# Kernel optimization log

Hardware: AMD Instinct MI355X
Metric: run time of the kernel (lower is better)

The kernel has to match this reference:

```python
import jax, jax.numpy as jnp
import numpy as np

N_STREAMS = 8
DIM = 1024
N_HEADS = 16
HEAD_DIM = DIM // N_HEADS
STREAM_DIM = DIM // N_STREAMS
EPS = 1e-6


def setup_inputs() -> dict:
    key = jax.random.key(0)
    ks = jax.random.split(key, 20)
    B, S, D = 2, 2048, DIM
    inp = {
        "x": jax.random.normal(ks[0], (B, S, D), jnp.float32),
        "rope_cos": jax.random.uniform(ks[1], (S, HEAD_DIM), jnp.float32),
        "rope_sin": jax.random.uniform(ks[2], (S, HEAD_DIM), jnp.float32),
        # DeltaOperator: learned per-channel decay logits
        "delta_decay": jax.random.normal(ks[3], (D,), jnp.float32) * 0.02,
        # gate_proj: Linear(D, 3*n)
        "gate_w": jax.random.normal(ks[4], (3 * N_STREAMS, D), jnp.float32) * 0.02,
        "gate_b": jnp.zeros((3 * N_STREAMS,), jnp.float32),
        "phi_res": jax.random.normal(ks[5], (N_STREAMS, N_STREAMS), jnp.float32) * 0.02,
        "ln1_w": jnp.ones((D,), jnp.float32),
        "ln2_w": jnp.ones((D,), jnp.float32),
        # MLP (StrategicLinear == Linear at inference)
        "w1": jax.random.normal(ks[6], (4 * D, D), jnp.float32) * 0.02,
        "b1": jnp.zeros((4 * D,), jnp.float32),
        "w2": jax.random.normal(ks[7], (D, 4 * D), jnp.float32) * 0.02,
        "b2": jnp.zeros((D,), jnp.float32),
        # nn.MultiheadAttention params
        "in_proj_w": jax.random.normal(ks[8], (3 * D, D), jnp.float32) * 0.02,
        "in_proj_b": jnp.zeros((3 * D,), jnp.float32),
        "out_w": jax.random.normal(ks[9], (D, D), jnp.float32) * 0.02,
        "out_b": jnp.zeros((D,), jnp.float32),
    }
    return inp


def delta_operator(x, decay_logits):
    # out_t = x_t - s_{t-1};  s_t = beta*s_{t-1} + (1-beta)*x_t  (per-channel EMA delta)
    beta = jax.nn.sigmoid(decay_logits)  # [D]

    def step(s, xt):
        out = xt - s
        s_new = beta * s + (1.0 - beta) * xt
        return s_new, out

    xT = jnp.swapaxes(x, 0, 1)  # [S,B,D]
    s0 = jnp.zeros_like(xT[0])
    _, ysT = jax.lax.scan(step, s0, xT)
    return jnp.swapaxes(ysT, 0, 1)  # [B,S,D]


def rms_norm(x, w):
    var = jnp.mean(x * x, axis=-1, keepdims=True)
    return x * jax.lax.rsqrt(var + EPS) * w


def sinkhorn_knopp(phi, iterations=15):
    K = jnp.exp(phi)
    for _ in range(iterations):
        K = K / jnp.sum(K, axis=1, keepdims=True)
        K = K / jnp.sum(K, axis=0, keepdims=True)
    return K


def causal_mha(x, in_proj_w, in_proj_b, out_w, out_b):
    B, S, D = x.shape
    qkv = x @ in_proj_w.T + in_proj_b  # [B,S,3D]
    q, k, v = jnp.split(qkv, 3, axis=-1)
    def heads(t):
        return t.reshape(B, S, N_HEADS, HEAD_DIM).transpose(0, 2, 1, 3)  # [B,H,S,hd]
    q, k, v = heads(q), heads(k), heads(v)
    scores = jnp.einsum("bhqd,bhkd->bhqk", q, k) / jnp.sqrt(jnp.float32(HEAD_DIM))
    mask = jnp.tril(jnp.ones((S, S), bool))
    scores = jnp.where(mask, scores, jnp.float32(-1e9))
    attn = jax.nn.softmax(scores, axis=-1)
    o = jnp.einsum("bhqk,bhkd->bhqd", attn, v)
    o = o.transpose(0, 2, 1, 3).reshape(B, S, D)
    return o @ out_w.T + out_b


def reference(x, rope_cos, rope_sin, delta_decay, gate_w, gate_b, phi_res,
              ln1_w, ln2_w, w1, b1, w2, b2, in_proj_w, in_proj_b, out_w, out_b):
    B, S, D = x.shape
    n = N_STREAMS
    x_delta = delta_operator(x, delta_decay)
    x_state = jnp.mean(x_delta, axis=1)  # [B,D]
    gates = x_state @ gate_w.T + gate_b  # [B,3n]
    g_res = jax.nn.sigmoid(gates[:, 2 * n:])[:, None, :, None]  # [B,1,n,1]
    H_res = sinkhorn_knopp(phi_res, 15)
    x_streams = x_delta.reshape(B, S, n, STREAM_DIM)
    # (x_perm @ H.T).permute back == einsum over stream axis
    mhc_out = jnp.einsum("bsnd,mn->bsmd", x_streams * g_res, H_res).reshape(B, S, D)
    normed = rms_norm(x_delta, ln1_w)
    attn_out = causal_mha(normed, in_proj_w, in_proj_b, out_w, out_b)
    normed2 = rms_norm(x_delta + attn_out, ln2_w)
    h = jax.nn.gelu(normed2 @ w1.T + b1, approximate=False)
    ffn_out = h @ w2.T + b2
    return x_delta + attn_out + ffn_out + mhc_out
```

## Files before the change

kernel.cpp:

```cpp
#include <hip/hip_runtime.h>
#include <hip/hip_bf16.h>
#include <math.h>

#define BB 2
#define SS 2048
#define DDIM 1024
#define NHEAD 16
#define NSTR 8
#define SDIMC 128
#define NCH 16
#define CLEN 128
#define EPSV 1e-6f

using bf16 = __hip_bfloat16;
typedef __attribute__((ext_vector_type(8))) __bf16 bf8;
typedef __attribute__((ext_vector_type(4))) __bf16 bf4v;
typedef __attribute__((ext_vector_type(4))) float f4;

__device__ __forceinline__ bf16 f2b(float v) { return __float2bfloat16(v); }
__device__ __forceinline__ bf8 ld8(const bf16* p) { return *(const bf8*)p; }
__device__ __forceinline__ f4 MFMA(bf8 a, bf8 b, f4 c) {
  return __builtin_amdgcn_mfma_f32_16x16x32_bf16(a, b, c, 0, 0, 0);
}
__device__ __forceinline__ float sigm(float x) { return 1.0f / (1.0f + expf(-x)); }
__device__ __forceinline__ float fexp2(float x) { return __builtin_amdgcn_exp2f(x); }
__device__ __forceinline__ float max3f(float a, float b, float c) {
  return fmaxf(fmaxf(a, b), c);
}

__device__ __forceinline__ float gelu_f(float v) {
  float x = v * 0.70710678118654752f;
  float ax = fabsf(x);
  float t = __builtin_amdgcn_rcpf(1.0f + 0.3275911f * ax);
  float p = ((((1.061405429f * t - 1.453152027f) * t + 1.421413741f) * t
              - 0.284496736f) * t + 0.254829592f) * t;
  float e = 1.0f - p * fexp2(-ax * ax * 1.4426950408889634f);
  e = copysignf(e, x);
  return 0.5f * v * (1.0f + e);
}

__device__ __forceinline__ void glds16(bf16* l, const bf16* g) {
  __builtin_amdgcn_global_load_lds(
      (const __attribute__((address_space(1))) unsigned int*)g,
      (__attribute__((address_space(3))) unsigned int*)l, 16, 0, 0);
}

__global__ __launch_bounds__(256) void cvt_all(const float* __restrict__ ipw,
                                               const float* __restrict__ ow,
                                               const float* __restrict__ w1,
                                               const float* __restrict__ w2,
                                               bf16* __restrict__ WIPW,
                                               bf16* __restrict__ WOW,
                                               bf16* __restrict__ W1B,
                                               bf16* __restrict__ W2B) {
  const int S1 = 3 * DDIM * DDIM, S2 = S1 + DDIM * DDIM,
            S3 = S2 + 4 * DDIM * DDIM;
  int i4 = (blockIdx.x * 256 + threadIdx.x) * 4;
  const float* src;
  bf16* dst;
  int off;
  if (i4 < S1)      { src = ipw; dst = WIPW; off = i4; }
  else if (i4 < S2) { src = ow;  dst = WOW;  off = i4 - S1; }
  else if (i4 < S3) { src = w1;  dst = W1B;  off = i4 - S2; }
  else              { src = w2;  dst = W2B;  off = i4 - S3; }
  float4 v = *(const float4*)(src + off);
  bf4v o;
  o[0] = (__bf16)v.x; o[1] = (__bf16)v.y; o[2] = (__bf16)v.z; o[3] = (__bf16)v.w;
  *(bf4v*)(dst + off) = o;
}

__global__ __launch_bounds__(256) void delta_passA(const float* __restrict__ x,
                                                   const float* __restrict__ decay,
                                                   float* __restrict__ SA) {
  int idx = blockIdx.x * 256 + threadIdx.x;
  int d = idx % DDIM;
  int c = (idx / DDIM) % NCH;
  int b = idx / (DDIM * NCH);
  float beta = sigm(decay[d]);
  float omb = 1.0f - beta;
  const float* xp = x + ((size_t)(b * SS + c * CLEN)) * DDIM + d;
  float s = 0.0f;
  for (int j = 0; j < CLEN; j++) {
    float xv = xp[(size_t)j * DDIM];
    s = beta * s + omb * xv;
  }
  SA[idx] = s;
}

__global__ __launch_bounds__(256) void delta_passB(const float* __restrict__ SA,
                                                   const float* __restrict__ decay,
                                                   float* __restrict__ SIN) {
  int idx = blockIdx.x * 256 + threadIdx.x;
  int d = idx % DDIM;
  int b = idx / DDIM;
  float beta = sigm(decay[d]);
  float p = beta;
  for (int i = 0; i < 7; i++) p *= p;
  float s = 0.0f;
  for (int c = 0; c < NCH; c++) {
    SIN[(b * NCH + c) * DDIM + d] = s;
    s = p * s + SA[(b * NCH + c) * DDIM + d];
  }
}

__global__ __launch_bounds__(256) void delta_passC(const float* __restrict__ x,
                                                   const float* __restrict__ decay,
                                                   const float* __restrict__ SIN,
                                                   float* __restrict__ XD,
                                                   float* __restrict__ SA) {
  int idx = blockIdx.x * 256 + threadIdx.x;
  int d = idx % DDIM;
  int c = (idx / DDIM) % NCH;
  int b = idx / (DDIM * NCH);
  float beta = sigm(decay[d]);
  float omb = 1.0f - beta;
  const float* xp = x + ((size_t)(b * SS + c * CLEN)) * DDIM + d;
  float* xdp = XD + ((size_t)(b * SS + c * CLEN)) * DDIM + d;
  float s = SIN[idx];
  float sum = 0.0f;
  for (int j = 0; j < CLEN; j++) {
    float xv = xp[(size_t)j * DDIM];
    float o = xv - s;
    xdp[(size_t)j * DDIM] = o;
    sum += o;
    s = beta * s + omb * xv;
  }
  SA[idx] = sum;
}

__global__ __launch_bounds__(1024) void gates_sinkhorn(const float* __restrict__ SA,
                                                       const float* __restrict__ gw,
                                                       const float* __restrict__ gb,
                                                       const float* __restrict__ phi,
                                                       float* __restrict__ gres,
                                                       float* __restrict__ hres) {
  int tid = threadIdx.x;
  int wave = tid >> 6, lane = tid & 63;
  int b = wave >> 3, j = wave & 7;
  float acc = 0.0f;
  for (int d = lane; d < DDIM; d += 64) {
    float xs = 0.0f;
    for (int c = 0; c < NCH; c++) xs += SA[(b * NCH + c) * DDIM + d];
    xs *= (1.0f / (float)SS);
    acc += xs * gw[(2 * NSTR + j) * DDIM + d];
  }
  for (int off = 32; off > 0; off >>= 1) acc += __shfl_down(acc, off);
  if (lane == 0) gres[b * NSTR + j] = sigm(acc + gb[2 * NSTR + j]);
  __syncthreads();
  if (tid == 0) {
    float Km[8][8];
    for (int i = 0; i < 8; i++)
      for (int jj = 0; jj < 8; jj++) Km[i][jj] = expf(phi[i * 8 + jj]);
    for (int it = 0; it < 15; it++) {
      for (int i = 0; i < 8; i++) {
        float rs = 0.0f;
        for (int jj = 0; jj < 8; jj++) rs += Km[i][jj];
        float inv = 1.0f / rs;
        for (int jj = 0; jj < 8; jj++) Km[i][jj] *= inv;
      }
      for (int jj = 0; jj < 8; jj++) {
        float cs = 0.0f;
        for (int i = 0; i < 8; i++) cs += Km[i][jj];
        float inv = 1.0f / cs;
        for (int i = 0; i < 8; i++) Km[i][jj] *= inv;
      }
    }
    for (int i = 0; i < 8; i++)
      for (int jj = 0; jj < 8; jj++) hres[i * 8 + jj] = Km[i][jj];
  }
}

__global__ __launch_bounds__(256) void rmsnorm_k(const float* __restrict__ in,
                                                 const float* __restrict__ w,
                                                 bf16* __restrict__ out) {
  int row = blockIdx.x;
  const float* r = in + (size_t)row * DDIM;
  int tid = threadIdx.x;
  float ss = 0.0f;
  for (int i = tid; i < DDIM; i += 256) {
    float v = r[i];
    ss += v * v;
  }
  for (int off = 32; off > 0; off >>= 1) ss += __shfl_down(ss, off);
  __shared__ float red[4];
  if ((tid & 63) == 0) red[tid >> 6] = ss;
  __syncthreads();
  float tot = red[0] + red[1] + red[2] + red[3];
  float sc = rsqrtf(tot / (float)DDIM + EPSV);
  bf16* o = out + (size_t)row * DDIM;
  for (int i = tid; i < DDIM; i += 256) o[i] = f2b(r[i] * sc * w[i]);
}

template <int EPI>
__global__ __launch_bounds__(512, 2) void gemm256(const bf16* __restrict__ Ag,
                                                  const bf16* __restrict__ Wg,
                                                  const float* __restrict__ bias,
                                                  bf16* __restrict__ outp,
                                                  int M, int N, int K, int nby) {
  __shared__ __align__(16) bf16 As[2][16384];
  __shared__ __align__(16) bf16 Bs[2][16384];
  int nwg = gridDim.x;
  int cpx = nwg >> 3;
  int l = (blockIdx.x & 7) * cpx + (blockIdx.x >> 3);
  int bm = l / nby, bn = l % nby;
  int m0 = bm * 256, n0 = bn * 256;
  int tid = threadIdx.x;
  int lane = tid & 63, wv = tid >> 6;
  int ml = lane & 15, quad = lane >> 4;
  int wrow = wv >> 2, wcol = wv & 3;

  size_t aoff[2][2], boff[2][2];
  int lof[2][2];
#pragma unroll
  for (int h = 0; h < 2; h++)
#pragma unroll
    for (int j = 0; j < 2; j++) {
      int b = tid * 16 + j * 8192;
      int s = b >> 10, w = b & 1023;
      int wl = w ^ (((w >> 9) & 1) << 5);
      int row = h * 128 + (s >> 1) * 16 + (wl >> 6);
      int col = (s & 1) * 32 + ((wl & 63) >> 1);
      aoff[h][j] = (size_t)(m0 + row) * K + col;
      boff[h][j] = (size_t)(n0 + row) * K + col;
      lof[h][j] = (h * 16384 + b) >> 1;
    }
  int wq2 = ((((ml << 6) + (quad << 4)) ^ (((int)(ml >= 8)) << 5))) >> 1;

#define SA_(c, kt, h) { glds16(&As[c][lof[h][0]], Ag + aoff[h][0] + (size_t)(kt) * 64); \
                        glds16(&As[c][lof[h][1]], Ag + aoff[h][1] + (size_t)(kt) * 64); }
#define SB_(c, kt, h) { glds16(&Bs[c][lof[h][0]], Wg + boff[h][0] + (size_t)(kt) * 64); \
                        glds16(&Bs[c][lof[h][1]], Wg + boff[h][1] + (size_t)(kt) * 64); }

  SA_(0, 0, 0); SA_(0, 0, 1);
  SB_(0, 0, 0); SB_(0, 0, 1);
  SB_(1, 1, 0); SB_(1, 1, 1);
  f4 acc[8][4] = {};
  asm volatile("s_waitcnt vmcnt(4)" ::: "memory");
  __builtin_amdgcn_s_barrier();
  asm volatile("" ::: "memory");

  int T = K >> 6;
  for (int t = 0; t < T; t++) {
    int c = t & 1;
    bf8 bfrag[4][2];
#pragma unroll
    for (int q = 0; q < 4; q++) {
      bf8 af[2][2];
#pragma unroll
      for (int mi2 = 0; mi2 < 2; mi2++)
#pragma unroll
        for (int kk = 0; kk < 2; kk++)
          af[mi2][kk] =
              ld8(&As[c][(((wrow * 8 + q * 2 + mi2) * 2 + kk) << 9) + wq2]);
      if (q == 0) {
#pragma unroll
        for (int ni = 0; ni < 4; ni++)
#pragma unroll
          for (int kk = 0; kk < 2; kk++)
            bfrag[ni][kk] =
                ld8(&Bs[c][(((wcol * 4 + ni) * 2 + kk) << 9) + wq2]);
      }
      if (q == 0 && t + 1 < T) SA_(c ^ 1, t + 1, 0);
      if (q == 1 && t + 1 < T) SA_(c ^ 1, t + 1, 1);
      if (q == 2 && t + 2 < T) SB_(c, t + 2, 0);
      if (q == 3 && t + 2 < T) SB_(c, t + 2, 1);
      __builtin_amdgcn_s_barrier();
      asm volatile("s_waitcnt lgkmcnt(0)" ::: "memory");
      __builtin_amdgcn_s_setprio(1);
#pragma unroll
      for (int mi2 = 0; mi2 < 2; mi2++)
#pragma unroll
        for (int ni = 0; ni < 4; ni++)
#pragma unroll
          for (int kk = 0; kk < 2; kk++)
            acc[q * 2 + mi2][ni] =
                MFMA(af[mi2][kk], bfrag[ni][kk], acc[q * 2 + mi2][ni]);
      __builtin_amdgcn_s_setprio(0);
      if (q == 3) {
        if (t + 2 < T) {
          asm volatile("s_waitcnt vmcnt(4)" ::: "memory");
        } else if (t + 1 < T) {
          asm volatile("s_waitcnt vmcnt(0)" ::: "memory");
        }
      }
      __builtin_amdgcn_s_barrier();
      asm volatile("" ::: "memory");
    }
  }
#pragma unroll
  for (int mi = 0; mi < 8; mi++)
#pragma unroll
    for (int ni = 0; ni < 4; ni++)
#pragma unroll
      for (int r = 0; r < 4; r++) {
        int row = m0 + wrow * 128 + mi * 16 + quad * 4 + r;
        int col = n0 + wcol * 64 + ni * 16 + ml;
        float v = acc[mi][ni][r] + bias[col];
        if (EPI == 1) v = gelu_f(v);
        outp[(size_t)row * N + col] = f2b(v);
      }
#undef SA_
#undef SB_
}

__global__ __launch_bounds__(512, 2) void gemm256sk(const bf16* __restrict__ Ag,
                                                    const bf16* __restrict__ Wg,
                                                    bf16* __restrict__ P01,
                                                    bf16* __restrict__ P23,
                                                    int M, int N, int K, int LDK,
                                                    int nby) {
  __shared__ __align__(16) bf16 As[2][16384];
  __shared__ __align__(16) bf16 Bs[2][16384];
  int nwg = gridDim.x;
  int cpx = nwg >> 3;
  int l = (blockIdx.x & 7) * cpx + (blockIdx.x >> 3);
  int nper = nwg >> 2;
  int sk = l / nper;
  int idx = l % nper;
  int bm = idx / nby, bn = idx % nby;
  int m0 = bm * 256, n0 = bn * 256;
  bf16* outp = (sk < 2) ? (P01 + (size_t)sk * M * N)
                        : (P23 + (size_t)(sk - 2) * M * N);
  int kbase = sk * K;
  int tid = threadIdx.x;
  int lane = tid & 63, wv = tid >> 6;
  int ml = lane & 15, quad = lane >> 4;
  int wrow = wv >> 2, wcol = wv & 3;

  size_t aoff[2][2], boff[2][2];
  int lof[2][2];
#pragma unroll
  for (int h = 0; h < 2; h++)
#pragma unroll
    for (int j = 0; j < 2; j++) {
      int b = tid * 16 + j * 8192;
      int s = b >> 10, w = b & 1023;
      int wl = w ^ (((w >> 9) & 1) << 5);
      int row = h * 128 + (s >> 1) * 16 + (wl >> 6);
      int col = (s & 1) * 32 + ((wl & 63) >> 1);
      aoff[h][j] = (size_t)(m0 + row) * LDK + kbase + col;
      boff[h][j] = (size_t)(n0 + row) * LDK + kbase + col;
      lof[h][j] = (h * 16384 + b) >> 1;
    }
  int wq2 = ((((ml << 6) + (quad << 4)) ^ (((int)(ml >= 8)) << 5))) >> 1;

#define SA_(c, kt, h) { glds16(&As[c][lof[h][0]], Ag + aoff[h][0] + (size_t)(kt) * 64); \
                        glds16(&As[c][lof[h][1]], Ag + aoff[h][1] + (size_t)(kt) * 64); }
#define SB_(c, kt, h) { glds16(&Bs[c][lof[h][0]], Wg + boff[h][0] + (size_t)(kt) * 64); \
                        glds16(&Bs[c][lof[h][1]], Wg + boff[h][1] + (size_t)(kt) * 64); }

  SA_(0, 0, 0); SA_(0, 0, 1);
  SB_(0, 0, 0); SB_(0, 0, 1);
  SB_(1, 1, 0); SB_(1, 1, 1);
  f4 acc[8][4] = {};
  asm volatile("s_waitcnt vmcnt(4)" ::: "memory");
  __builtin_amdgcn_s_barrier();
  asm volatile("" ::: "memory");

  int T = K >> 6;
  for (int t = 0; t < T; t++) {
    int c = t & 1;
    bf8 bfrag[4][2];
#pragma unroll
    for (int q = 0; q < 4; q++) {
      bf8 af[2][2];
#pragma unroll
      for (int mi2 = 0; mi2 < 2; mi2++)
#pragma unroll
        for (int kk = 0; kk < 2; kk++)
          af[mi2][kk] =
              ld8(&As[c][(((wrow * 8 + q * 2 + mi2) * 2 + kk) << 9) + wq2]);
      if (q == 0) {
#pragma unroll
        for (int ni = 0; ni < 4; ni++)
#pragma unroll
          for (int kk = 0; kk < 2; kk++)
            bfrag[ni][kk] =
                ld8(&Bs[c][(((wcol * 4 + ni) * 2 + kk) << 9) + wq2]);
      }
      if (q == 0 && t + 1 < T) SA_(c ^ 1, t + 1, 0);
      if (q == 1 && t + 1 < T) SA_(c ^ 1, t + 1, 1);
      if (q == 2 && t + 2 < T) SB_(c, t + 2, 0);
      if (q == 3 && t + 2 < T) SB_(c, t + 2, 1);
      __builtin_amdgcn_s_barrier();
      asm volatile("s_waitcnt lgkmcnt(0)" ::: "memory");
      __builtin_amdgcn_s_setprio(1);
#pragma unroll
      for (int mi2 = 0; mi2 < 2; mi2++)
#pragma unroll
        for (int ni = 0; ni < 4; ni++)
#pragma unroll
          for (int kk = 0; kk < 2; kk++)
            acc[q * 2 + mi2][ni] =
                MFMA(af[mi2][kk], bfrag[ni][kk], acc[q * 2 + mi2][ni]);
      __builtin_amdgcn_s_setprio(0);
      if (q == 3) {
        if (t + 2 < T) {
          asm volatile("s_waitcnt vmcnt(4)" ::: "memory");
        } else if (t + 1 < T) {
          asm volatile("s_waitcnt vmcnt(0)" ::: "memory");
        }
      }
      __builtin_amdgcn_s_barrier();
      asm volatile("" ::: "memory");
    }
  }
#pragma unroll
  for (int mi = 0; mi < 8; mi++)
#pragma unroll
    for (int ni = 0; ni < 4; ni++)
#pragma unroll
      for (int r = 0; r < 4; r++) {
        int row = m0 + wrow * 128 + mi * 16 + quad * 4 + r;
        int col = n0 + wcol * 64 + ni * 16 + ml;
        outp[(size_t)row * N + col] = f2b(acc[mi][ni][r]);
      }
#undef SA_
#undef SB_
}

template <int ODT, int EPI>
__global__ __launch_bounds__(256) void gemm_lds64(const bf16* __restrict__ A,
                                                  const bf16* __restrict__ W,
                                                  const float* __restrict__ bias,
                                                  const float* __restrict__ res,
                                                  void* __restrict__ outp,
                                                  int M, int N, int K) {
  __shared__ bf16 As[2][64 * 32];
  __shared__ bf16 Bs[2][128 * 32];
  int tid = threadIdx.x;
  int lane = tid & 63, wv = tid >> 6;
  int ml = lane & 15, quad = lane >> 4;
  int wr = wv & 1, wc = wv >> 1;
  int m0 = blockIdx.x * 64, n0 = blockIdx.y * 128;
  const bf16* gaA;
  const bf16* gb[2];
  int lofA, lofs[2];
  {
    int c = tid;
    int row = c >> 2, kc = (c & 3) * 8;
    gaA = A + (size_t)(m0 + row) * K + kc;
    lofA = c * 8;
  }
#pragma unroll
  for (int it = 0; it < 2; it++) {
    int c = it * 256 + tid;
    int row = c >> 2, kc = (c & 3) * 8;
    gb[it] = W + (size_t)(n0 + row) * K + kc;
    lofs[it] = c * 8;
  }
  glds16(&As[0][lofA], gaA);
#pragma unroll
  for (int it = 0; it < 2; it++) glds16(&Bs[0][lofs[it]], gb[it]);
  f4 acc[2][4] = {};
  int nk = K >> 5;
  int cur = 0;
  __syncthreads();
  for (int t = 0; t < nk; t++) {
    if (t + 1 < nk) {
      int ko = (t + 1) * 32;
      glds16(&As[cur ^ 1][lofA], gaA + ko);
#pragma unroll
      for (int it = 0; it < 2; it++) glds16(&Bs[cur ^ 1][lofs[it]], gb[it] + ko);
    }
    bf8 af[2], bfr[4];
#pragma unroll
    for (int mi = 0; mi < 2; mi++)
      af[mi] = ld8(&As[cur][(wr * 32 + mi * 16 + ml) * 32 + quad * 8]);
#pragma unroll
    for (int ni = 0; ni < 4; ni++)
      bfr[ni] = ld8(&Bs[cur][(wc * 64 + ni * 16 + ml) * 32 + quad * 8]);
#pragma unroll
    for (int mi = 0; mi < 2; mi++)
#pragma unroll
      for (int ni = 0; ni < 4; ni++)
        acc[mi][ni] = MFMA(af[mi], bfr[ni], acc[mi][ni]);
    __syncthreads();
    cur ^= 1;
  }
#pragma unroll
  for (int mi = 0; mi < 2; mi++)
#pragma unroll
    for (int ni = 0; ni < 4; ni++)
#pragma unroll
      for (int r = 0; r < 4; r++) {
        int row = m0 + wr * 32 + mi * 16 + quad * 4 + r;
        int col = n0 + wc * 64 + ni * 16 + ml;
        size_t idx = (size_t)row * N + col;
        float v = acc[mi][ni][r] + bias[col];
        if (EPI == 1) v = gelu_f(v);
        if (EPI == 2) v += res[idx];
        if (ODT == 1) ((bf16*)outp)[idx] = f2b(v);
        else ((float*)outp)[idx] = v;
      }
}

__global__ __launch_bounds__(256) void vtrans(const bf16* __restrict__ qkv,
                                              bf16* __restrict__ VT) {
  int bid = blockIdx.x;
  int st = bid % (SS / 64);
  int h = (bid / (SS / 64)) % NHEAD;
  int b = bid / ((SS / 64) * NHEAD);
  __shared__ bf16 tile[64][65];
  int s0 = st * 64;
  int tid = threadIdx.x;
  for (int it = 0; it < 16; it++) {
    int sl = it * 4 + (tid >> 6), dl = tid & 63;
    tile[sl][dl] = qkv[(size_t)(b * SS + s0 + sl) * (3 * DDIM) + 2 * DDIM + h * 64 + dl];
  }
  __syncthreads();
  for (int it = 0; it < 16; it++) {
    int dl = it * 4 + (tid >> 6), sl = tid & 63;
    VT[((size_t)(b * NHEAD + h) * 64 + dl) * SS + s0 + sl] = tile[sl][dl];
  }
}

__device__ __forceinline__ void qk_softmax(bool active, int kt, int q0, int nkt,
                                           const bf8 kf[4][2], const bf8* qf,
                                           f4* oacc, float& m, float& l,
                                           bf8* pf, bf16 (*pl)[72],
                                           int ml, int quad, int k0) {
  if (!active) return;
  const float SC = 0.125f * 1.44269504089f;
  f4 s[4] = {{0,0,0,0},{0,0,0,0},{0,0,0,0},{0,0,0,0}};
  __builtin_amdgcn_s_setprio(1);
#pragma unroll
  for (int kk = 0; kk < 2; kk++)
#pragma unroll
    for (int c = 0; c < 4; c++)
      s[c] = MFMA(kf[c][kk], qf[kk], s[c]);
  __builtin_amdgcn_s_setprio(0);
  if (kt == nkt - 1) {
    int qi = q0 + ml;
#pragma unroll
    for (int c = 0; c < 4; c++)
#pragma unroll
      for (int r = 0; r < 4; r++)
        if (k0 + c * 16 + quad * 4 + r > qi) s[c][r] = -1e30f;
  }
  float mx = max3f(s[0][0], s[0][1], s[0][2]);
  mx = max3f(mx, s[0][3], s[1][0]);
  mx = max3f(mx, s[1][1], s[1][2]);
  mx = max3f(mx, s[1][3], s[2][0]);
  mx = max3f(mx, s[2][1], s[2][2]);
  mx = max3f(mx, s[2][3], s[3][0]);
  mx = max3f(mx, s[3][1], s[3][2]);
  mx = fmaxf(mx, s[3][3]);
  mx = fmaxf(mx, __shfl_xor(mx, 16));
  mx = fmaxf(mx, __shfl_xor(mx, 32));
  float mxs = mx * SC;
  float p[4][4];
  float rs = 0.0f;
  if (__all(mxs - m <= 8.0f)) {
#pragma unroll
    for (int c = 0; c < 4; c++)
#pragma unroll
      for (int r = 0; r < 4; r++) {
        p[c][r] = fexp2(__builtin_fmaf(s[c][r], SC, -m));
        rs += p[c][r];
      }
    rs += __shfl_xor(rs, 16);
    rs += __shfl_xor(rs, 32);
    l += rs;
  } else {
    float mn = fmaxf(m, mxs);
    float alpha = fexp2(m - mn);
#pragma unroll
    for (int c = 0; c < 4; c++)
#pragma unroll
      for (int r = 0; r < 4; r++) {
        p[c][r] = fexp2(__builtin_fmaf(s[c][r], SC, -mn));
        rs += p[c][r];
      }
    rs += __shfl_xor(rs, 16);
    rs += __shfl_xor(rs, 32);
    l = l * alpha + rs;
    m = mn;
    float alr[4];
#pragma unroll
    for (int r = 0; r < 4; r++) alr[r] = __shfl(alpha, quad * 4 + r);
#pragma unroll
    for (int c = 0; c < 4; c++)
#pragma unroll
      for (int r = 0; r < 4; r++) oacc[c][r] *= alr[r];
  }
#pragma unroll
  for (int c = 0; c < 4; c++) {
    bf4v w;
#pragma unroll
    for (int r = 0; r < 4; r++) w[r] = (__bf16)p[c][r];
    *(bf4v*)&pl[ml][c * 16 + quad * 4] = w;
  }
#pragma unroll
  for (int kk = 0; kk < 2; kk++) pf[kk] = ld8(&pl[ml][kk * 32 + quad * 8]);
}

__device__ __forceinline__ void pv_acc(bool active, const bf8* pf,
                                       const bf8 vf[4][2], f4* oacc) {
  if (!active) return;
  __builtin_amdgcn_s_setprio(1);
#pragma unroll
  for (int c = 0; c < 4; c++)
#pragma unroll
    for (int kk = 0; kk < 2; kk++)
      oacc[c] = MFMA(pf[kk], vf[c][kk], oacc[c]);
  __builtin_amdgcn_s_setprio(0);
}

__global__ __launch_bounds__(256) void flash_attn(const bf16* __restrict__ qkv,
                                                  const bf16* __restrict__ VT,
                                                  bf16* __restrict__ obuf) {
  int rb = blockIdx.x;
  int slot = rb >> 3;
  int bid = (rb & 7) * 64 + slot;
  int j = slot & 15;
  int blk = (slot & 32) ? (15 - j) : j;
  int h = (bid >> 4) & 15;
  int b = bid >> 8;
  int tid = threadIdx.x;
  int wv = tid >> 6, lane = tid & 63;
  int ml = lane & 15, quad = lane >> 4;
  int idx0 = blk * 4 + wv;
  int idx1 = 127 - idx0;
  int q0a = idx0 * 16, q0b = idx1 * 16;
  int nkt0 = blk + 1;
  int nkt1 = 32 - blk;
  int maxn = nkt1;

  __shared__ __align__(16) bf16 Ks[2][64 * 64];
  __shared__ __align__(16) bf16 Vs[2][64 * 64];
  __shared__ __align__(16) bf16 plds[4][2][16][72];
  bf16 (*plA)[72] = plds[wv][0];
  bf16 (*plB)[72] = plds[wv][1];

  bf8 qfa[2], qfb[2];
#pragma unroll
  for (int kk = 0; kk < 2; kk++) {
    qfa[kk] = ld8(qkv + (size_t)(b * SS + q0a + ml) * (3 * DDIM) + h * 64 + kk * 32 + quad * 8);
    qfb[kk] = ld8(qkv + (size_t)(b * SS + q0b + ml) * (3 * DDIM) + h * 64 + kk * 32 + quad * 8);
  }
  f4 oacca[4] = {{0,0,0,0},{0,0,0,0},{0,0,0,0},{0,0,0,0}};
  f4 oaccb[4] = {{0,0,0,0},{0,0,0,0},{0,0,0,0},{0,0,0,0}};
  float ma = -1e30f, la = 0.0f, mb = -1e30f, lb = 0.0f;

  const bf16* kglob = qkv + (size_t)b * SS * (3 * DDIM) + DDIM + h * 64;
  const bf16* vglob = VT + (size_t)(b * NHEAD + h) * 64 * SS;

#pragma unroll
  for (int it = 0; it < 2; it++) {
    int lam = it * 256 + tid;
    int row = lam >> 3;
    int ch = (lam & 7) ^ (row & 7);
    glds16(&Ks[0][lam * 8], kglob + (size_t)row * (3 * DDIM) + ch * 8);
    glds16(&Vs[0][lam * 8], vglob + (size_t)row * SS + ch * 8);
  }
  __syncthreads();
  int cur = 0;
  for (int kt = 0; kt < maxn; kt++) {
    int k0 = kt * 64;
    if (kt + 1 < maxn) {
      int k0n = (kt + 1) * 64;
#pragma unroll
      for (int it = 0; it < 2; it++) {
        int lam = it * 256 + tid;
        int row = lam >> 3;
        int ch = (lam & 7) ^ (row & 7);
        glds16(&Ks[cur ^ 1][lam * 8], kglob + (size_t)(k0n + row) * (3 * DDIM) + ch * 8);
        glds16(&Vs[cur ^ 1][lam * 8], vglob + (size_t)row * SS + k0n + ch * 8);
      }
    }
    bool act0 = kt < nkt0;
    bf8 kf[4][2];
#pragma unroll
    for (int kk = 0; kk < 2; kk++)
#pragma unroll
      for (int c = 0; c < 4; c++) {
        int chunk = ((c * 16 + ml) << 3) + ((kk * 4 + quad) ^ (ml & 7));
        kf[c][kk] = ld8(&Ks[cur][chunk * 8]);
      }
    bf8 pfa[2], pfb[2];
    qk_softmax(act0, kt, q0a, nkt0, kf, qfa, oacca, ma, la, pfa, plA, ml, quad, k0);
    qk_softmax(true, kt, q0b, nkt1, kf, qfb, oaccb, mb, lb, pfb, plB, ml, quad, k0);
    bf8 vf[4][2];
#pragma unroll
    for (int kk = 0; kk < 2; kk++)
#pragma unroll
      for (int c = 0; c < 4; c++) {
        int chunk = ((c * 16 + ml) << 3) + ((kk * 4 + quad) ^ (ml & 7));
        vf[c][kk] = ld8(&Vs[cur][chunk * 8]);
      }
    pv_acc(act0, pfa, vf, oacca);
    pv_acc(true, pfb, vf, oaccb);
    __syncthreads();
    cur ^= 1;
  }
  float lna[4], lnb[4];
#pragma unroll
  for (int r = 0; r < 4; r++) {
    lna[r] = __shfl(la, quad * 4 + r);
    lnb[r] = __shfl(lb, quad * 4 + r);
  }
#pragma unroll
  for (int c = 0; c < 4; c++)
#pragma unroll
    for (int r = 0; r < 4; r++) {
      int rowa = q0a + quad * 4 + r;
      int rowb = q0b + quad * 4 + r;
      obuf[(size_t)(b * SS + rowa) * DDIM + h * 64 + c * 16 + ml] =
          f2b(oacca[c][r] / lna[r]);
      obuf[(size_t)(b * SS + rowb) * DDIM + h * 64 + c * 16 + ml] =
          f2b(oaccb[c][r] / lnb[r]);
    }
}

__global__ __launch_bounds__(256) void final_k(const float* __restrict__ y,
                                               const bf16* __restrict__ P0,
                                               const bf16* __restrict__ P1,
                                               const bf16* __restrict__ P2,
                                               const bf16* __restrict__ P3,
                                               const float* __restrict__ bias,
                                               const float* __restrict__ xd,
                                               const float* __restrict__ hres,
                                               const float* __restrict__ gres,
                                               float* __restrict__ out) {
  int row = blockIdx.x;
  int b = row / SS;
  int tid = threadIdx.x;
  __shared__ float cf[8][8];
  if (tid < 64) cf[tid >> 3][tid & 7] = hres[tid] * gres[b * NSTR + (tid & 7)];
  __syncthreads();
  int i4 = tid * 4;
  int m = i4 >> 7, dd = i4 & 127;
  size_t base = (size_t)row * DDIM + i4;
  f4 vy = *(const f4*)(y + base);
  f4 vb = *(const f4*)(bias + i4);
  bf4v p0 = *(const bf4v*)(P0 + base);
  bf4v p1 = *(const bf4v*)(P1 + base);
  bf4v p2 = *(const bf4v*)(P2 + base);
  bf4v p3 = *(const bf4v*)(P3 + base);
  const float* xr = xd + (size_t)row * DDIM;
  float acc[4];
#pragma unroll
  for (int jj = 0; jj < 4; jj++)
    acc[jj] = vy[jj] + vb[jj] + (float)p0[jj] + (float)p1[jj] +
              (float)p2[jj] + (float)p3[jj];
#pragma unroll
  for (int n = 0; n < 8; n++) {
    f4 vx = *(const f4*)(xr + n * SDIMC + dd);
#pragma unroll
    for (int jj = 0; jj < 4; jj++) acc[jj] += cf[m][n] * vx[jj];
  }
  f4 vo = {acc[0], acc[1], acc[2], acc[3]};
  *(f4*)(out + base) = vo;
}

extern "C" void kernel_launch(void* const* d_in, const int* in_sizes, int n_in,
                              void* d_out, int out_size, void* d_ws, size_t ws_size,
                              hipStream_t stream) {
  const float* x     = (const float*)d_in[0];
  const float* decay = (const float*)d_in[3];
  const float* gw    = (const float*)d_in[4];
  const float* gb    = (const float*)d_in[5];
  const float* phi   = (const float*)d_in[6];
  const float* ln1   = (const float*)d_in[7];
  const float* ln2   = (const float*)d_in[8];
  const float* w1    = (const float*)d_in[9];
  const float* b1    = (const float*)d_in[10];
  const float* w2    = (const float*)d_in[11];
  const float* b2    = (const float*)d_in[12];
  const float* ipw   = (const float*)d_in[13];
  const float* ipb   = (const float*)d_in[14];
  const float* ow    = (const float*)d_in[15];
  const float* obs   = (const float*)d_in[16];
  float* out = (float*)d_out;

  const size_t MB = 1048576ull;
  char* wsp = (char*)d_ws;
  float* SA   = (float*)(wsp);
  float* SIN  = (float*)(wsp + 131072ull);
  float* GRES = (float*)(wsp + 262144ull);
  float* HRES = (float*)(wsp + 262208ull);
  float* XD   = (float*)(wsp + 1 * MB);
  float* AO   = (float*)(wsp + 17 * MB);
  bf16*  NORM = (bf16*)(wsp + 33 * MB);
  bf16*  OB   = (bf16*)(wsp + 41 * MB);
  bf16*  QKV  = (bf16*)(wsp + 49 * MB);
  bf16*  VT   = (bf16*)(wsp + 73 * MB);
  bf16*  HB   = (bf16*)(wsp + 49 * MB);
  bf16*  WIPW = (bf16*)(wsp + 81 * MB);
  bf16*  WOW  = (bf16*)(wsp + 87 * MB);
  bf16*  W1B  = (bf16*)(wsp + 89 * MB);
  bf16*  W2B  = (bf16*)(wsp + 97 * MB);
  bf16* PKB0 = (bf16*)(wsp + 33 * MB);
  bf16* PKB2 = (bf16*)(wsp + 81 * MB);

  cvt_all<<<dim3(12 * DDIM * DDIM / 1024), dim3(256), 0, stream>>>(
      ipw, ow, w1, w2, WIPW, WOW, W1B, W2B);

  delta_passA<<<dim3(BB * NCH * DDIM / 256), dim3(256), 0, stream>>>(x, decay, SA);
  delta_passB<<<dim3(BB * DDIM / 256), dim3(256), 0, stream>>>(SA, decay, SIN);
  delta_passC<<<dim3(BB * NCH * DDIM / 256), dim3(256), 0, stream>>>(x, decay, SIN, XD, SA);
  gates_sinkhorn<<<dim3(1), dim3(1024), 0, stream>>>(SA, gw, gb, phi, GRES, HRES);
  rmsnorm_k<<<dim3(BB * SS), dim3(256), 0, stream>>>(XD, ln1, NORM);
  gemm256<0><<<dim3(192), dim3(512), 0, stream>>>(NORM, WIPW, ipb, QKV,
                                                  BB * SS, 3 * DDIM, DDIM, 12);
  vtrans<<<dim3(BB * NHEAD * (SS / 64)), dim3(256), 0, stream>>>(QKV, VT);
  flash_attn<<<dim3(BB * NHEAD * 16), dim3(256), 0, stream>>>(QKV, VT, OB);
  gemm_lds64<0, 2><<<dim3(64, 8), dim3(256), 0, stream>>>(OB, WOW, obs, XD,
                                                          AO, BB * SS, DDIM, DDIM);
  rmsnorm_k<<<dim3(BB * SS), dim3(256), 0, stream>>>(AO, ln2, NORM);
  gemm256<1><<<dim3(256), dim3(512), 0, stream>>>(NORM, W1B, b1, HB,
                                                  BB * SS, 4 * DDIM, DDIM, 16);
  gemm256sk<<<dim3(256), dim3(512), 0, stream>>>(HB, W2B, PKB0, PKB2,
                                                 BB * SS, DDIM, DDIM, 4 * DDIM, 4);
  final_k<<<dim3(BB * SS), dim3(256), 0, stream>>>(
      AO, PKB0, PKB0 + (size_t)BB * SS * DDIM, PKB2,
      PKB2 + (size_t)BB * SS * DDIM, b2, XD, HRES, GRES, out);
}
```

Baseline: 399.6 us.

## Split flash-attention query tiles across 8 waves instead of two per wave

The flash attention kernel now launches 512 threads per block, and each wave owns a single 16-row query tile instead of two paired tiles (a short causal tile and its long mirror). Waves in the first half go idle once their causal range ends, while the block keeps loading K/V tiles for the second half. Each thread now loads one chunk per K/V tile instead of two. This roughly halves per-wave register pressure and doubles wave-level parallelism, at the cost of load imbalance between the two halves and more waves competing at each block barrier.

```diff
diff --git a/kernel.cpp b/kernel.cpp
--- a/kernel.cpp
+++ b/kernel.cpp
@@ -515,12 +515,11 @@
   }
 }
 
-__device__ __forceinline__ void qk_softmax(bool active, int kt, int q0, int nkt,
+__device__ __forceinline__ void qk_softmax(int kt, int q0, int nkt,
                                            const bf8 kf[4][2], const bf8* qf,
                                            f4* oacc, float& m, float& l,
                                            bf8* pf, bf16 (*pl)[72],
                                            int ml, int quad, int k0) {
-  if (!active) return;
   const float SC = 0.125f * 1.44269504089f;
   f4 s[4] = {{0,0,0,0},{0,0,0,0},{0,0,0,0},{0,0,0,0}};
   __builtin_amdgcn_s_setprio(1);
@@ -595,21 +594,9 @@
   for (int kk = 0; kk < 2; kk++) pf[kk] = ld8(&pl[ml][kk * 32 + quad * 8]);
 }
 
-__device__ __forceinline__ void pv_acc(bool active, const bf8* pf,
-                                       const bf8 vf[4][2], f4* oacc) {
-  if (!active) return;
-  __builtin_amdgcn_s_setprio(1);
-#pragma unroll
-  for (int c = 0; c < 4; c++)
-#pragma unroll
-    for (int kk = 0; kk < 2; kk++)
-      oacc[c] = MFMA(pf[kk], vf[c][kk], oacc[c]);
-  __builtin_amdgcn_s_setprio(0);
-}
-
-__global__ __launch_bounds__(256) void flash_attn(const bf16* __restrict__ qkv,
-                                                  const bf16* __restrict__ VT,
-                                                  bf16* __restrict__ obuf) {
+__global__ __launch_bounds__(512, 4) void flash_attn(const bf16* __restrict__ qkv,
+                                                     const bf16* __restrict__ VT,
+                                                     bf16* __restrict__ obuf) {
   int rb = blockIdx.x;
   int slot = rb >> 3;
   int bid = (rb & 7) * 64 + slot;
@@ -620,35 +607,29 @@
   int tid = threadIdx.x;
   int wv = tid >> 6, lane = tid & 63;
   int ml = lane & 15, quad = lane >> 4;
-  int idx0 = blk * 4 + wv;
-  int idx1 = 127 - idx0;
-  int q0a = idx0 * 16, q0b = idx1 * 16;
-  int nkt0 = blk + 1;
-  int nkt1 = 32 - blk;
-  int maxn = nkt1;
+  int half = wv >> 2, sub = wv & 3;
+  int idx = half ? (127 - (blk * 4 + sub)) : (blk * 4 + sub);
+  int q0 = idx * 16;
+  int nkt = half ? (32 - blk) : (blk + 1);
+  int maxn = 32 - blk;
 
   __shared__ __align__(16) bf16 Ks[2][64 * 64];
   __shared__ __align__(16) bf16 Vs[2][64 * 64];
-  __shared__ __align__(16) bf16 plds[4][2][16][72];
-  bf16 (*plA)[72] = plds[wv][0];
-  bf16 (*plB)[72] = plds[wv][1];
-
-  bf8 qfa[2], qfb[2];
-#pragma unroll
-  for (int kk = 0; kk < 2; kk++) {
-    qfa[kk] = ld8(qkv + (size_t)(b * SS + q0a + ml) * (3 * DDIM) + h * 64 + kk * 32 + quad * 8);
-    qfb[kk] = ld8(qkv + (size_t)(b * SS + q0b + ml) * (3 * DDIM) + h * 64 + kk * 32 + quad * 8);
-  }
-  f4 oacca[4] = {{0,0,0,0},{0,0,0,0},{0,0,0,0},{0,0,0,0}};
-  f4 oaccb[4] = {{0,0,0,0},{0,0,0,0},{0,0,0,0},{0,0,0,0}};
-  float ma = -1e30f, la = 0.0f, mb = -1e30f, lb = 0.0f;
+  __shared__ __align__(16) bf16 plds[8][16][72];
+  bf16 (*pl)[72] = plds[wv];
+
+  bf8 qf[2];
+#pragma unroll
+  for (int kk = 0; kk < 2; kk++)
+    qf[kk] = ld8(qkv + (size_t)(b * SS + q0 + ml) * (3 * DDIM) + h * 64 + kk * 32 + quad * 8);
+  f4 oacc[4] = {{0,0,0,0},{0,0,0,0},{0,0,0,0},{0,0,0,0}};
+  float m = -1e30f, l = 0.0f;
 
   const bf16* kglob = qkv + (size_t)b * SS * (3 * DDIM) + DDIM + h * 64;
   const bf16* vglob = VT + (size_t)(b * NHEAD + h) * 64 * SS;
 
-#pragma unroll
-  for (int it = 0; it < 2; it++) {
-    int lam = it * 256 + tid;
+  {
+    int lam = tid;
     int row = lam >> 3;
     int ch = (lam & 7) ^ (row & 7);
     glds16(&Ks[0][lam * 8], kglob + (size_t)row * (3 * DDIM) + ch * 8);
@@ -660,56 +641,52 @@
     int k0 = kt * 64;
     if (kt + 1 < maxn) {
       int k0n = (kt + 1) * 64;
-#pragma unroll
-      for (int it = 0; it < 2; it++) {
-        int lam = it * 256 + tid;
-        int row = lam >> 3;
-        int ch = (lam & 7) ^ (row & 7);
-        glds16(&Ks[cur ^ 1][lam * 8], kglob + (size_t)(k0n + row) * (3 * DDIM) + ch * 8);
-        glds16(&Vs[cur ^ 1][lam * 8], vglob + (size_t)row * SS + k0n + ch * 8);
-      }
-    }
-    bool act0 = kt < nkt0;
-    bf8 kf[4][2];
-#pragma unroll
-    for (int kk = 0; kk < 2; kk++)
-#pragma unroll
-      for (int c = 0; c < 4; c++) {
-        int chunk = ((c * 16 + ml) << 3) + ((kk * 4 + quad) ^ (ml & 7));
-        kf[c][kk] = ld8(&Ks[cur][chunk * 8]);
-      }
-    bf8 pfa[2], pfb[2];
-    qk_softmax(act0, kt, q0a, nkt0, kf, qfa, oacca, ma, la, pfa, plA, ml, quad, k0);
-    qk_softmax(true, kt, q0b, nkt1, kf, qfb, oaccb, mb, lb, pfb, plB, ml, quad, k0);
-    bf8 vf[4][2];
-#pragma unroll
-    for (int kk = 0; kk < 2; kk++)
-#pragma unroll
-      for (int c = 0; c < 4; c++) {
-        int chunk = ((c * 16 + ml) << 3) + ((kk * 4 + quad) ^ (ml & 7));
-        vf[c][kk] = ld8(&Vs[cur][chunk * 8]);
-      }
-    pv_acc(act0, pfa, vf, oacca);
-    pv_acc(true, pfb, vf, oaccb);
+      int lam = tid;
+      int row = lam >> 3;
+      int ch = (lam & 7) ^ (row & 7);
+      glds16(&Ks[cur ^ 1][lam * 8], kglob + (size_t)(k0n + row) * (3 * DDIM) + ch * 8);
+      glds16(&Vs[cur ^ 1][lam * 8], vglob + (size_t)row * SS + k0n + ch * 8);
+    }
+    if (kt < nkt) {
+      bf8 kf[4][2];
+#pragma unroll
+      for (int kk = 0; kk < 2; kk++)
+#pragma unroll
+        for (int c = 0; c < 4; c++) {
+          int chunk = ((c * 16 + ml) << 3) + ((kk * 4 + quad) ^ (ml & 7));
+          kf[c][kk] = ld8(&Ks[cur][chunk * 8]);
+        }
+      bf8 pf[2];
+      qk_softmax(kt, q0, nkt, kf, qf, oacc, m, l, pf, pl, ml, quad, k0);
+      bf8 vf[4][2];
+#pragma unroll
+      for (int kk = 0; kk < 2; kk++)
+#pragma unroll
+        for (int c = 0; c < 4; c++) {
+          int chunk = ((c * 16 + ml) << 3) + ((kk * 4 + quad) ^ (ml & 7));
+          vf[c][kk] = ld8(&Vs[cur][chunk * 8]);
+        }
+      __builtin_amdgcn_s_setprio(1);
+#pragma unroll
+      for (int c = 0; c < 4; c++)
+#pragma unroll
+        for (int kk = 0; kk < 2; kk++)
+          oacc[c] = MFMA(pf[kk], vf[c][kk], oacc[c]);
+      __builtin_amdgcn_s_setprio(0);
+    }
     __syncthreads();
     cur ^= 1;
   }
-  float lna[4], lnb[4];
-#pragma unroll
-  for (int r = 0; r < 4; r++) {
-    lna[r] = __shfl(la, quad * 4 + r);
-    lnb[r] = __shfl(lb, quad * 4 + r);
-  }
+  float ln[4];
+#pragma unroll
+  for (int r = 0; r < 4; r++) ln[r] = __shfl(l, quad * 4 + r);
 #pragma unroll
   for (int c = 0; c < 4; c++)
 #pragma unroll
     for (int r = 0; r < 4; r++) {
-      int rowa = q0a + quad * 4 + r;
-      int rowb = q0b + quad * 4 + r;
-      obuf[(size_t)(b * SS + rowa) * DDIM + h * 64 + c * 16 + ml] =
-          f2b(oacca[c][r] / lna[r]);
-      obuf[(size_t)(b * SS + rowb) * DDIM + h * 64 + c * 16 + ml] =
-          f2b(oaccb[c][r] / lnb[r]);
+      int row = q0 + quad * 4 + r;
+      obuf[(size_t)(b * SS + row) * DDIM + h * 64 + c * 16 + ml] =
+          f2b(oacc[c][r] / ln[r]);
     }
 }
 
@@ -805,7 +782,7 @@
   gemm256<0><<<dim3(192), dim3(512), 0, stream>>>(NORM, WIPW, ipb, QKV,
                                                   BB * SS, 3 * DDIM, DDIM, 12);
   vtrans<<<dim3(BB * NHEAD * (SS / 64)), dim3(256), 0, stream>>>(QKV, VT);
-  flash_attn<<<dim3(BB * NHEAD * 16), dim3(256), 0, stream>>>(QKV, VT, OB);
+  flash_attn<<<dim3(BB * NHEAD * 16), dim3(512), 0, stream>>>(QKV, VT, OB);
   gemm_lds64<0, 2><<<dim3(64, 8), dim3(256), 0, stream>>>(OB, WOW, obs, XD,
                                                           AO, BB * SS, DDIM, DDIM);
   rmsnorm_k<<<dim3(BB * SS), dim3(256), 0, stream>>>(AO, ln2, NORM);
```

After: 402.1 us, median of 2. Within noise of the previous version (+0.6%).
